# Kernel optimization log

Hardware: AMD Instinct MI355X
Metric: run time of the kernel (lower is better)

The kernel has to match this reference:

```python
import jax, jax.numpy as jnp
import numpy as np


def setup_inputs() -> dict:
    key = jax.random.key(0)
    k1, k2 = jax.random.split(key)
    B, C, H, W = 4, 256, 64, 64
    f_m = jax.random.normal(k1, (B, C, H, W), dtype=jnp.float32)
    f_d = jax.random.normal(k2, (B, C, H, W), dtype=jnp.float32)
    return {"f_m": f_m, "f_d": f_d}


def reference(f_m, f_d):
    B, C, H, W = f_d.shape
    HW = H * W
    f_fuse = f_m + f_d                      # [B, C, H, W]
    f_c = f_fuse.reshape(B, C, HW)          # [B, C, HW]
    # scores[b, n, m] = sum_c f_c[b, c, n] * f_c[b, c, m]
    scores = jnp.einsum('bcn,bcm->bnm', f_c, f_c)   # [B, HW, HW]
    att = jax.nn.softmax(scores, axis=-1)           # softmax over last dim
    f_d_r = f_d.reshape(B, C, HW)                   # [B, C, HW]
    # out[b, c, m] = sum_n f_d_r[b, c, n] * att[b, n, m]
    f_d_att = jnp.einsum('bcn,bnm->bcm', f_d_r, att).reshape(B, C, H, W)
    return f_d_att + f_d
```

## Files before the change

kernel.cpp:

```cpp
#include <hip/hip_runtime.h>
#include <math.h>

#define B_ 4
#define C_ 256
#define N_ 4096
#define LDE 68
#define LDX 72

typedef __attribute__((ext_vector_type(8))) short short8;
typedef __attribute__((ext_vector_type(4))) float f32x4;
typedef __attribute__((ext_vector_type(2))) float f32x2;

__device__ inline ushort f2bf(float f) {
    uint u = __float_as_uint(f);
    return (ushort)((u + 0x7fffu + ((u >> 16) & 1u)) >> 16);
}
__device__ inline float bf2f(ushort h) { return __uint_as_float(((uint)h) << 16); }

__device__ inline f32x4 mfma16(short8 a, short8 b, f32x4 c) {
    return __builtin_amdgcn_mfma_f32_16x16x32_bf16(a, b, c, 0, 0, 0);
}
__device__ inline f32x4 mfma8(long a, long b, f32x4 c) {
    return __builtin_amdgcn_mfma_f32_16x16x32_fp8_fp8(a, b, c, 0, 0, 0);
}

__device__ inline size_t xfi8(int b, int nt, int kk) {
    return (((size_t)(b * 256 + nt)) * 8 + kk) * 512;
}
__device__ inline size_t ffi(int b, int nc, int ct, int k2) {
    return ((((size_t)(b * 64 + nc)) * 16 + ct) * 2 + k2) * 512;
}
__device__ inline size_t eti(int b, int mt, int ng) {
    return (((size_t)(b * 256 + mt)) * 512 + (size_t)ng) * 128;
}
__device__ inline size_t zmi(int b, int nc, int mt) {
    return ((size_t)(b * 64 + nc)) * 256 + mt;
}

__global__ __launch_bounds__(256) void prep_x_kernel(const float* __restrict__ fm,
                                                     const float* __restrict__ fd,
                                                     uchar* __restrict__ xfrag8) {
    __shared__ ushort xl[64][LDX];
    const int b = blockIdx.z, c0 = blockIdx.y * 64, n0 = blockIdx.x * 64;
    const int t = threadIdx.x;
    const int n4 = (t & 15) * 4, cl = t >> 4;
    const size_t base = (size_t)b * C_ * N_;
    #pragma unroll
    for (int p = 0; p < 4; ++p) {
        const int cr = 16 * p + cl;
        const float4 m4 = *(const float4*)(fm + base + (size_t)(c0 + cr) * N_ + n0 + n4);
        const float4 d4 = *(const float4*)(fd + base + (size_t)(c0 + cr) * N_ + n0 + n4);
        ushort4 xo;
        xo.x = f2bf(m4.x + d4.x); xo.y = f2bf(m4.y + d4.y);
        xo.z = f2bf(m4.z + d4.z); xo.w = f2bf(m4.w + d4.w);
        *(ushort4*)(&xl[cr][n4]) = xo;
    }
    __syncthreads();
    const int l = t & 63, tl = t >> 6;
    const int nl = 16 * tl + (l & 15);
    #pragma unroll
    for (int j = 0; j < 2; ++j) {
        const int kk = (c0 >> 5) + j;
        const int cb = 32 * j + 8 * (l >> 4);
        float f[8];
        #pragma unroll
        for (int i = 0; i < 8; ++i) f[i] = bf2f(xl[cb + i][nl]);
        int d0 = __builtin_amdgcn_cvt_pk_fp8_f32(f[0], f[1], 0, 0);
        d0 = __builtin_amdgcn_cvt_pk_fp8_f32(f[2], f[3], d0, 1);
        int d1 = __builtin_amdgcn_cvt_pk_fp8_f32(f[4], f[5], 0, 0);
        d1 = __builtin_amdgcn_cvt_pk_fp8_f32(f[6], f[7], d1, 1);
        uint* dst = (uint*)(xfrag8 + xfi8(b, (n0 >> 4) + tl, kk) + (size_t)l * 8);
        dst[0] = (uint)d0; dst[1] = (uint)d1;
    }
}

__global__ __launch_bounds__(512, 2) void lsum_t_kernel(const uchar* __restrict__ xfrag8,
                                                        uchar* __restrict__ E8,
                                                        uchar* __restrict__ zmask,
                                                        float* __restrict__ rsbase,
                                                        float* __restrict__ rsadd,
                                                        float* __restrict__ dgall) {
    __shared__ float red[8][64];
    __shared__ float dgl[64];
    __shared__ uchar chl[34];
    __shared__ int cnt_s;
    __shared__ uint zst[34];
    const int bid = blockIdx.x;
    const int b = (bid >> 1) & 3;
    const int n0 = ((((bid >> 3) << 1) | (bid & 1))) * 64;
    const int j = n0 >> 6;
    const int t = threadIdx.x, lane = t & 63, w = t >> 6;
    const int l15 = lane & 15, q = lane >> 4;
    const int g = w >> 2, wm = w & 3;

    if (t == 0) {
        int c = 0;
        chl[c++] = (uchar)j;
        for (int k = 0; k < 64; ++k) {
            if (k == j) continue;
            const bool own = (k > j) ? (((j + k) & 1) == 0) : (((j + k) & 1) == 1);
            if (own) chl[c++] = (uchar)k;
        }
        cnt_s = c;
    }
    if (t < 34) zst[t] = 0u;

    long af[4][8];
    #pragma unroll
    for (int ns = 0; ns < 4; ++ns)
        #pragma unroll
        for (int kk = 0; kk < 8; ++kk)
            af[ns][kk] = *(const long*)(xfrag8 + xfi8(b, (n0 >> 4) + ns, kk) + (size_t)lane * 8);

    float dv[4][4];
    #pragma unroll
    for (int ns = 0; ns < 4; ++ns) {
        f32x4 dacc = {0.f, 0.f, 0.f, 0.f};
        #pragma unroll
        for (int kk = 0; kk < 8; ++kk)
            dacc = mfma8(af[ns][kk], af[ns][kk], dacc);
        #pragma unroll
        for (int r = 0; r < 4; ++r)
            dv[ns][r] = __shfl(dacc[r], 20 * q + r, 64);
    }
    if (w == 0 && l15 == 0) {
        #pragma unroll
        for (int ns = 0; ns < 4; ++ns)
            #pragma unroll
            for (int r = 0; r < 4; ++r)
                dgl[16 * ns + 4 * q + r] = dv[ns][r];
    }

    __syncthreads();
    const int cnt = cnt_s;

    long bn[8];
    {
        const int mt0 = 4 * (int)chl[g] + wm;
        #pragma unroll
        for (int kk = 0; kk < 8; ++kk)
            bn[kk] = *(const long*)(xfrag8 + xfi8(b, mt0, kk) + (size_t)lane * 8);
    }
    const size_t ebl = (size_t)l15 * 8 + 4 * (q & 1);
    const int ngb = (n0 >> 3) + (q >> 1);

    float rs[4][4] = {};
    for (int it = 0; it < 17; ++it) {
        const int idx = 2 * it + g;
        const bool valid = idx < cnt;
        const int kc = chl[valid ? idx : 0];
        const int mt = 4 * kc + wm;
        int idxn = 2 * (it + 1) + g; if (idxn >= cnt) idxn = 0;
        const int mtn = 4 * (int)chl[idxn] + wm;

        f32x4 a0 = {0.f,0.f,0.f,0.f}, a1 = {0.f,0.f,0.f,0.f};
        f32x4 a2 = {0.f,0.f,0.f,0.f}, a3 = {0.f,0.f,0.f,0.f};
        float dg0 = 0.f, dg1 = 0.f, dg2 = 0.f, dg3 = 0.f;
        __builtin_amdgcn_s_setprio(1);
        #pragma unroll
        for (int kk = 0; kk < 8; ++kk) {
            const long bc = bn[kk];
            a0 = mfma8(af[0][kk], bc, a0);
            a1 = mfma8(af[1][kk], bc, a1);
            a2 = mfma8(af[2][kk], bc, a2);
            a3 = mfma8(af[3][kk], bc, a3);
            bn[kk] = *(const long*)(xfrag8 + xfi8(b, mtn, kk) + (size_t)lane * 8);
            const uint lo = (uint)(unsigned long)bc;
            const uint hi = (uint)((unsigned long)bc >> 32);
            const f32x2 p0 = __builtin_amdgcn_cvt_pk_f32_fp8((int)lo, false);
            const f32x2 p1 = __builtin_amdgcn_cvt_pk_f32_fp8((int)lo, true);
            const f32x2 p2 = __builtin_amdgcn_cvt_pk_f32_fp8((int)hi, false);
            const f32x2 p3 = __builtin_amdgcn_cvt_pk_f32_fp8((int)hi, true);
            dg0 = fmaf(p0.x, p0.x, dg0); dg0 = fmaf(p0.y, p0.y, dg0);
            dg1 = fmaf(p1.x, p1.x, dg1); dg1 = fmaf(p1.y, p1.y, dg1);
            dg2 = fmaf(p2.x, p2.x, dg2); dg2 = fmaf(p2.y, p2.y, dg2);
            dg3 = fmaf(p3.x, p3.x, dg3); dg3 = fmaf(p3.y, p3.y, dg3);
        }
        __builtin_amdgcn_s_setprio(0);

        float df[4][4];
#define EDF(AA, NS)                                                    \
        df[NS][0] = AA[0] - dv[NS][0]; df[NS][1] = AA[1] - dv[NS][1];  \
        df[NS][2] = AA[2] - dv[NS][2]; df[NS][3] = AA[3] - dv[NS][3];
        EDF(a0, 0) EDF(a1, 1) EDF(a2, 2) EDF(a3, 3)
#undef EDF
        const float mxA = fmaxf(
            fmaxf(fmaxf(fmaxf(df[0][0], df[0][1]), fmaxf(df[0][2], df[0][3])),
                  fmaxf(fmaxf(df[1][0], df[1][1]), fmaxf(df[1][2], df[1][3]))),
            fmaxf(fmaxf(fmaxf(df[2][0], df[2][1]), fmaxf(df[2][2], df[2][3])),
                  fmaxf(fmaxf(df[3][0], df[3][1]), fmaxf(df[3][2], df[3][3]))));
        const bool nzA = valid && (__ballot(mxA > -30.0f) != 0ULL);
        if (valid && lane == 0) zmask[zmi(b, j, mt)] = nzA ? 1 : 0;
        if (nzA) {
            uint dpk[4];
#define EEXP(NS)                                                                       \
            {                                                                          \
                float e0 = __expf(df[NS][0]), e1 = __expf(df[NS][1]);                  \
                float e2 = __expf(df[NS][2]), e3 = __expf(df[NS][3]);                  \
                rs[NS][0] += e0; rs[NS][1] += e1; rs[NS][2] += e2; rs[NS][3] += e3;    \
                int d = __builtin_amdgcn_cvt_pk_fp8_f32(e0, e1, 0, 0);                 \
                d = __builtin_amdgcn_cvt_pk_fp8_f32(e2, e3, d, 1);                     \
                dpk[NS] = (uint)d;                                                     \
            }
            EEXP(0) EEXP(1) EEXP(2) EEXP(3)
#undef EEXP
            #pragma unroll
            for (int ns = 0; ns < 4; ++ns)
                *(uint*)(E8 + eti(b, mt, ngb + 2 * ns) + ebl) = dpk[ns];
        }
        if (valid && kc != j) {
            float dgm = dg0 + dg1 + dg2 + dg3;
            dgm += __shfl_xor(dgm, 16, 64);
            dgm += __shfl_xor(dgm, 32, 64);
            float dfB[4][4];
            #pragma unroll
            for (int ns = 0; ns < 4; ++ns) {
                dfB[ns][0] = (ns==0?a0[0]:ns==1?a1[0]:ns==2?a2[0]:a3[0]) - dgm;
                dfB[ns][1] = (ns==0?a0[1]:ns==1?a1[1]:ns==2?a2[1]:a3[1]) - dgm;
                dfB[ns][2] = (ns==0?a0[2]:ns==1?a1[2]:ns==2?a2[2]:a3[2]) - dgm;
                dfB[ns][3] = (ns==0?a0[3]:ns==1?a1[3]:ns==2?a2[3]:a3[3]) - dgm;
            }
            uint bits = 0;
            #pragma unroll
            for (int ns = 0; ns < 4; ++ns) {
                const float m2 = fmaxf(fmaxf(dfB[ns][0], dfB[ns][1]),
                                       fmaxf(dfB[ns][2], dfB[ns][3]));
                if (__ballot(m2 > -30.0f) != 0ULL) bits |= (1u << ns);
            }
            if (bits) {
                if (lane == 0) atomicOr(&zst[idx], bits);
                float cs = 0.f;
                #pragma unroll
                for (int ns = 0; ns < 4; ++ns)
                    #pragma unroll
                    for (int r = 0; r < 4; ++r)
                        cs += __expf(dfB[ns][r]);
                cs += __shfl_xor(cs, 16, 64);
                cs += __shfl_xor(cs, 32, 64);
                if (q == 0) atomicAdd(rsadd + b * N_ + 16 * mt + l15, cs);
            }
        }
    }
    #pragma unroll
    for (int off = 1; off < 16; off <<= 1)
        #pragma unroll
        for (int ns = 0; ns < 4; ++ns)
            #pragma unroll
            for (int r = 0; r < 4; ++r)
                rs[ns][r] += __shfl_xor(rs[ns][r], off, 64);
    if (l15 == 0) {
        #pragma unroll
        for (int ns = 0; ns < 4; ++ns)
            #pragma unroll
            for (int r = 0; r < 4; ++r)
                red[w][16 * ns + 4 * q + r] = rs[ns][r];
    }
    __syncthreads();
    if (t < 64) {
        float s = 0.f;
        #pragma unroll
        for (int ww = 0; ww < 8; ++ww) s += red[ww][t];
        rsbase[b * N_ + n0 + t] = s;
        dgall[b * N_ + n0 + t] = dgl[t];
    }
    if (t >= 64 && t < 64 + 33 * 4) {
        const int ii = (t - 64) >> 2, ns = (t - 64) & 3;
        const int idx = ii + 1;
        if (idx < cnt) {
            const int kc = chl[idx];
            zmask[zmi(b, kc, 4 * j + ns)] = (((zst[idx] >> ns) & 1u) != 0u) ? 2 : 0;
        }
    }
}

__global__ __launch_bounds__(512, 2) void out_e_kernel(const uchar* __restrict__ E8,
                                                       const uchar* __restrict__ zmask,
                                                       const float* __restrict__ rsbase,
                                                       const float* __restrict__ rsadd,
                                                       const float* __restrict__ dgall,
                                                       const uchar* __restrict__ xfrag8,
                                                       const float* __restrict__ fd32,
                                                       float* __restrict__ outp) {
    __shared__ ushort esc[8][16][66];
    const int bid = blockIdx.x;
    const int b = (bid >> 1) & 3;
    const int m0 = ((((bid >> 3) << 1) | (bid & 1))) * 64;
    const int t = threadIdx.x, lane = t & 63, w = t >> 6;
    const int l15 = lane & 15, q = lane >> 4;
    const size_t fb = (size_t)b * C_ * N_;
    const uchar* mrow = zmask + zmi(b, 0, m0 >> 4);

    f32x4 acc[2][4];
    #pragma unroll
    for (int ct = 0; ct < 2; ++ct)
        #pragma unroll
        for (int mt = 0; mt < 4; ++mt)
            acc[ct][mt] = (f32x4){0.f, 0.f, 0.f, 0.f};

    for (int gg = 0; gg < 8; ++gg) {
        uint mk[8];
        #pragma unroll
        for (int i = 0; i < 8; ++i)
            mk[i] = *(const uint*)(mrow + (size_t)(8 * gg + i) * 256);
        #pragma unroll
        for (int i = 0; i < 8; ++i) {
            const uint mki = mk[i];
            if (mki == 0) continue;
            const int nc = 8 * gg + i;
            const float* rb = rsbase + b * N_ + 64 * nc + 8 * q;
            const float* ra = rsadd + b * N_ + 64 * nc + 8 * q;
            float4 s0[2], s1[2];
            #pragma unroll
            for (int k2 = 0; k2 < 2; ++k2) {
                const float4 b0 = *(const float4*)(rb + 32 * k2);
                const float4 b1 = *(const float4*)(rb + 32 * k2 + 4);
                const float4 a0v = *(const float4*)(ra + 32 * k2);
                const float4 a1v = *(const float4*)(ra + 32 * k2 + 4);
                s0[k2].x = 1.0f / (b0.x + a0v.x); s0[k2].y = 1.0f / (b0.y + a0v.y);
                s0[k2].z = 1.0f / (b0.z + a0v.z); s0[k2].w = 1.0f / (b0.w + a0v.w);
                s1[k2].x = 1.0f / (b1.x + a1v.x); s1[k2].y = 1.0f / (b1.y + a1v.y);
                s1[k2].z = 1.0f / (b1.z + a1v.z); s1[k2].w = 1.0f / (b1.w + a1v.w);
            }
            short8 fn[2][2];
            #pragma unroll
            for (int ct = 0; ct < 2; ++ct) {
                const int c = 32 * w + 16 * ct + l15;
                const float* frow = fd32 + fb + (size_t)c * N_ + 64 * nc + 8 * q;
                #pragma unroll
                for (int k2 = 0; k2 < 2; ++k2) {
                    const float4 fa = *(const float4*)(frow + 32 * k2);
                    const float4 fb4 = *(const float4*)(frow + 32 * k2 + 4);
                    union { ushort us[8]; short8 v; } u;
                    u.us[0] = f2bf(fa.x * s0[k2].x); u.us[1] = f2bf(fa.y * s0[k2].y);
                    u.us[2] = f2bf(fa.z * s0[k2].z); u.us[3] = f2bf(fa.w * s0[k2].w);
                    u.us[4] = f2bf(fb4.x * s1[k2].x); u.us[5] = f2bf(fb4.y * s1[k2].y);
                    u.us[6] = f2bf(fb4.z * s1[k2].z); u.us[7] = f2bf(fb4.w * s1[k2].w);
                    fn[ct][k2] = u.v;
                }
            }
            if ((mki & ~0x01010101u) == 0u) {
                #pragma unroll
                for (int k2 = 0; k2 < 2; ++k2) {
                    #pragma unroll
                    for (int mt = 0; mt < 4; ++mt) {
                        if (((mki >> (8 * mt)) & 0xffu) != 1u) continue;
                        const long e8 = *(const long*)(E8 + eti(b, (m0 >> 4) + mt, 8 * nc + 4 * k2 + q) + (size_t)l15 * 8);
                        const uint lo = (uint)(unsigned long)e8;
                        const uint hi = (uint)((unsigned long)e8 >> 32);
                        const f32x2 f01 = __builtin_amdgcn_cvt_pk_f32_fp8((int)lo, false);
                        const f32x2 f23 = __builtin_amdgcn_cvt_pk_f32_fp8((int)lo, true);
                        const f32x2 f45 = __builtin_amdgcn_cvt_pk_f32_fp8((int)hi, false);
                        const f32x2 f67 = __builtin_amdgcn_cvt_pk_f32_fp8((int)hi, true);
                        union { uint u[4]; short8 v; } be;
                        asm("v_cvt_pk_bf16_f32 %0, %1, %2" : "=v"(be.u[0]) : "v"(f01.x), "v"(f01.y));
                        asm("v_cvt_pk_bf16_f32 %0, %1, %2" : "=v"(be.u[1]) : "v"(f23.x), "v"(f23.y));
                        asm("v_cvt_pk_bf16_f32 %0, %1, %2" : "=v"(be.u[2]) : "v"(f45.x), "v"(f45.y));
                        asm("v_cvt_pk_bf16_f32 %0, %1, %2" : "=v"(be.u[3]) : "v"(f67.x), "v"(f67.y));
                        acc[0][mt] = mfma16(fn[0][k2], be.v, acc[0][mt]);
                        acc[1][mt] = mfma16(fn[1][k2], be.v, acc[1][mt]);
                    }
                }
            } else {
                #pragma unroll
                for (int mt = 0; mt < 4; ++mt) {
                    long bmf[8];
                    #pragma unroll
                    for (int kk = 0; kk < 8; ++kk)
                        bmf[kk] = *(const long*)(xfrag8 + xfi8(b, (m0 >> 4) + mt, kk) + (size_t)lane * 8);
                    #pragma unroll
                    for (int nt = 0; nt < 4; ++nt) {
                        long anf[8];
                        #pragma unroll
                        for (int kk = 0; kk < 8; ++kk)
                            anf[kk] = *(const long*)(xfrag8 + xfi8(b, 4 * nc + nt, kk) + (size_t)lane * 8);
                        f32x4 sacc = {0.f, 0.f, 0.f, 0.f};
                        #pragma unroll
                        for (int kk = 0; kk < 8; ++kk)
                            sacc = mfma8(anf[kk], bmf[kk], sacc);
                        #pragma unroll
                        for (int r = 0; r < 4; ++r) {
                            const float gv = dgall[b * N_ + 64 * nc + 16 * nt + 4 * q + r];
                            esc[w][l15][16 * nt + 4 * q + r] = f2bf(__expf(sacc[r] - gv));
                        }
                    }
                    #pragma unroll
                    for (int k2 = 0; k2 < 2; ++k2) {
                        const short8 be = *(const short8*)(&esc[w][l15][32 * k2 + 8 * q]);
                        acc[0][mt] = mfma16(fn[0][k2], be, acc[0][mt]);
                        acc[1][mt] = mfma16(fn[1][k2], be, acc[1][mt]);
                    }
                }
            }
        }
    }
    #pragma unroll
    for (int ct = 0; ct < 2; ++ct)
        #pragma unroll
        for (int mt = 0; mt < 4; ++mt)
            #pragma unroll
            for (int r = 0; r < 4; ++r) {
                const int c = 32 * w + 16 * ct + 4 * q + r;
                const int m = m0 + 16 * mt + l15;
                const size_t o = fb + (size_t)c * N_ + m;
                outp[o] = acc[ct][mt][r] + fd32[o];
            }
}

__global__ __launch_bounds__(256) void prep_kernel(const float* __restrict__ fm,
                                                   const float* __restrict__ fd,
                                                   uchar* __restrict__ xfrag8,
                                                   ushort* __restrict__ ffrag) {
    __shared__ ushort xl[64][LDX];
    __shared__ ushort fl[64][LDX];
    const int b = blockIdx.z, c0 = blockIdx.y * 64, n0 = blockIdx.x * 64;
    const int t = threadIdx.x;
    const int n4 = (t & 15) * 4, cl = t >> 4;
    const size_t base = (size_t)b * C_ * N_;
    #pragma unroll
    for (int p = 0; p < 4; ++p) {
        const int cr = 16 * p + cl;
        const float4 m4 = *(const float4*)(fm + base + (size_t)(c0 + cr) * N_ + n0 + n4);
        const float4 d4 = *(const float4*)(fd + base + (size_t)(c0 + cr) * N_ + n0 + n4);
        ushort4 fo;
        fo.x = f2bf(d4.x); fo.y = f2bf(d4.y); fo.z = f2bf(d4.z); fo.w = f2bf(d4.w);
        *(ushort4*)(&fl[cr][n4]) = fo;
        ushort4 xo;
        xo.x = f2bf(m4.x + d4.x); xo.y = f2bf(m4.y + d4.y);
        xo.z = f2bf(m4.z + d4.z); xo.w = f2bf(m4.w + d4.w);
        *(ushort4*)(&xl[cr][n4]) = xo;
    }
    __syncthreads();
    const int l = t & 63, tl = t >> 6;
    {
        const int nl = 16 * tl + (l & 15);
        #pragma unroll
        for (int j = 0; j < 2; ++j) {
            const int kk = (c0 >> 5) + j;
            const int cb = 32 * j + 8 * (l >> 4);
            float f[8];
            #pragma unroll
            for (int i = 0; i < 8; ++i) f[i] = bf2f(xl[cb + i][nl]);
            int d0 = __builtin_amdgcn_cvt_pk_fp8_f32(f[0], f[1], 0, 0);
            d0 = __builtin_amdgcn_cvt_pk_fp8_f32(f[2], f[3], d0, 1);
            int d1 = __builtin_amdgcn_cvt_pk_fp8_f32(f[4], f[5], 0, 0);
            d1 = __builtin_amdgcn_cvt_pk_fp8_f32(f[6], f[7], d1, 1);
            uint* dst = (uint*)(xfrag8 + xfi8(b, (n0 >> 4) + tl, kk) + (size_t)l * 8);
            dst[0] = (uint)d0; dst[1] = (uint)d1;
        }
    }
    {
        const int row = 16 * tl + (l & 15);
        #pragma unroll
        for (int k2 = 0; k2 < 2; ++k2) {
            const int col = 32 * k2 + 8 * (l >> 4);
            const ushort4 a0 = *(const ushort4*)(&fl[row][col]);
            const ushort4 a1 = *(const ushort4*)(&fl[row][col + 4]);
            ushort* dst = ffrag + ffi(b, n0 >> 6, (c0 >> 4) + tl, k2) + l * 8;
            *(ushort4*)(dst) = a0; *(ushort4*)(dst + 4) = a1;
        }
    }
}

__global__ __launch_bounds__(512, 2) void lsum_g_kernel(const uchar* __restrict__ xfrag8,
                                                        float* __restrict__ lg) {
    __shared__ float red[8][64];
    __shared__ float dgl[64];
    const int bid = blockIdx.x;
    const int b = (bid >> 1) & 3;
    const int n0 = ((((bid >> 3) << 1) | (bid & 1))) * 64;
    const int t = threadIdx.x, lane = t & 63, w = t >> 6;
    const int l15 = lane & 15, q = lane >> 4;

    long af[4][8];
    #pragma unroll
    for (int ns = 0; ns < 4; ++ns)
        #pragma unroll
        for (int kk = 0; kk < 8; ++kk)
            af[ns][kk] = *(const long*)(xfrag8 + xfi8(b, (n0 >> 4) + ns, kk) + (size_t)lane * 8);

    float dv[4][4];
    #pragma unroll
    for (int ns = 0; ns < 4; ++ns) {
        f32x4 dacc = {0.f, 0.f, 0.f, 0.f};
        #pragma unroll
        for (int kk = 0; kk < 8; ++kk)
            dacc = mfma8(af[ns][kk], af[ns][kk], dacc);
        #pragma unroll
        for (int r = 0; r < 4; ++r)
            dv[ns][r] = __shfl(dacc[r], 20 * q + r, 64);
    }
    if (w == 0 && l15 == 0) {
        #pragma unroll
        for (int ns = 0; ns < 4; ++ns)
            #pragma unroll
            for (int r = 0; r < 4; ++r)
                dgl[16 * ns + 4 * q + r] = dv[ns][r];
    }

    long bn[8];
    #pragma unroll
    for (int kk = 0; kk < 8; ++kk)
        bn[kk] = *(const long*)(xfrag8 + xfi8(b, w, kk) + (size_t)lane * 8);

    float rs[4][4] = {};
    for (int mc = 0; mc < 32; ++mc) {
        const int mtn = (mc + 1 < 32) ? (mc + 1) * 8 + w : w;
        f32x4 a0 = {0.f,0.f,0.f,0.f}, a1 = {0.f,0.f,0.f,0.f};
        f32x4 a2 = {0.f,0.f,0.f,0.f}, a3 = {0.f,0.f,0.f,0.f};
        #pragma unroll
        for (int kk = 0; kk < 8; ++kk) {
            const long bc = bn[kk];
            a0 = mfma8(af[0][kk], bc, a0);
            a1 = mfma8(af[1][kk], bc, a1);
            a2 = mfma8(af[2][kk], bc, a2);
            a3 = mfma8(af[3][kk], bc, a3);
            bn[kk] = *(const long*)(xfrag8 + xfi8(b, mtn, kk) + (size_t)lane * 8);
        }
        #pragma unroll
        for (int r = 0; r < 4; ++r) {
            rs[0][r] += __expf(a0[r] - dv[0][r]);
            rs[1][r] += __expf(a1[r] - dv[1][r]);
            rs[2][r] += __expf(a2[r] - dv[2][r]);
            rs[3][r] += __expf(a3[r] - dv[3][r]);
        }
    }
    #pragma unroll
    for (int off = 1; off < 16; off <<= 1)
        #pragma unroll
        for (int ns = 0; ns < 4; ++ns)
            #pragma unroll
            for (int r = 0; r < 4; ++r)
                rs[ns][r] += __shfl_xor(rs[ns][r], off, 64);
    if (l15 == 0) {
        #pragma unroll
        for (int ns = 0; ns < 4; ++ns)
            #pragma unroll
            for (int r = 0; r < 4; ++r)
                red[w][16 * ns + 4 * q + r] = rs[ns][r];
    }
    __syncthreads();
    if (t < 64) {
        float s = 0.f;
        #pragma unroll
        for (int ww = 0; ww < 8; ++ww) s += red[ww][t];
        lg[b * N_ + n0 + t] = dgl[t] + __logf(s);
    }
}

__global__ __launch_bounds__(512, 2) void out_g_kernel(const uchar* __restrict__ xfrag8,
                                                       const ushort* __restrict__ ffrag,
                                                       const float* __restrict__ gg,
                                                       const float* __restrict__ fd32,
                                                       float* __restrict__ outp) {
    __shared__ ushort ET[2][64][LDE];
    const int bid = blockIdx.x;
    const int b = (bid >> 1) & 3;
    const int m0 = ((((bid >> 3) << 1) | (bid & 1))) * 64;
    const int t = threadIdx.x, lane = t & 63, w = t >> 6;
    const int l15 = lane & 15, q = lane >> 4;
    const int a = w & 3, h = w >> 2;
    const size_t fb = (size_t)b * C_ * N_;

    long bfr[2][8];
    #pragma unroll
    for (int jt = 0; jt < 2; ++jt)
        #pragma unroll
        for (int kk = 0; kk < 8; ++kk)
            bfr[jt][kk] = *(const long*)(xfrag8 + xfi8(b, (m0 >> 4) + 2 * h + jt, kk) + (size_t)lane * 8);

    f32x4 acc[2][4];
    #pragma unroll
    for (int ct = 0; ct < 2; ++ct)
        #pragma unroll
        for (int mt = 0; mt < 4; ++mt)
            acc[ct][mt] = (f32x4){0.f, 0.f, 0.f, 0.f};

    long an[8];
    #pragma unroll
    for (int kk = 0; kk < 8; ++kk)
        an[kk] = *(const long*)(xfrag8 + xfi8(b, a, kk) + (size_t)lane * 8);
    float gn[4];
    #pragma unroll
    for (int r = 0; r < 4; ++r) gn[r] = gg[b * N_ + 16 * a + 4 * q + r];

    int p = 0;
    for (int n0c = 0; n0c < N_; n0c += 64, p ^= 1) {
        const int nc = n0c >> 6;
        short8 fn[2][2];
        #pragma unroll
        for (int ct = 0; ct < 2; ++ct)
            #pragma unroll
            for (int k2 = 0; k2 < 2; ++k2)
                fn[ct][k2] = *(const short8*)(ffrag + ffi(b, nc, 2 * w + ct, k2) + lane * 8);
        float gv[4];
        #pragma unroll
        for (int r = 0; r < 4; ++r) gv[r] = gn[r];
        const int nx = (n0c + 64 < N_) ? n0c + 64 : 0;
        #pragma unroll
        for (int r = 0; r < 4; ++r) gn[r] = gg[b * N_ + nx + 16 * a + 4 * q + r];

        f32x4 s0 = {0.f, 0.f, 0.f, 0.f}, s1 = {0.f, 0.f, 0.f, 0.f};
        #pragma unroll
        for (int kk = 0; kk < 8; ++kk) {
            s0 = mfma8(an[kk], bfr[0][kk], s0);
            s1 = mfma8(an[kk], bfr[1][kk], s1);
            an[kk] = *(const long*)(xfrag8 + xfi8(b, (nx >> 4) + a, kk) + (size_t)lane * 8);
        }
        ushort4 e0, e1;
        e0.x = f2bf(__expf(s0[0] - gv[0])); e0.y = f2bf(__expf(s0[1] - gv[1]));
        e0.z = f2bf(__expf(s0[2] - gv[2])); e0.w = f2bf(__expf(s0[3] - gv[3]));
        e1.x = f2bf(__expf(s1[0] - gv[0])); e1.y = f2bf(__expf(s1[1] - gv[1]));
        e1.z = f2bf(__expf(s1[2] - gv[2])); e1.w = f2bf(__expf(s1[3] - gv[3]));
        *(ushort4*)(&ET[p][32 * h + l15][16 * a + 4 * q])      = e0;
        *(ushort4*)(&ET[p][32 * h + 16 + l15][16 * a + 4 * q]) = e1;

        asm volatile("s_waitcnt lgkmcnt(0)\n\ts_barrier" ::: "memory");

        #pragma unroll
        for (int k2 = 0; k2 < 2; ++k2) {
            #pragma unroll
            for (int mt = 0; mt < 4; ++mt) {
                const short8 be = *(const short8*)(&ET[p][16 * mt + l15][32 * k2 + 8 * q]);
                acc[0][mt] = mfma16(fn[0][k2], be, acc[0][mt]);
                acc[1][mt] = mfma16(fn[1][k2], be, acc[1][mt]);
            }
        }
    }
    #pragma unroll
    for (int ct = 0; ct < 2; ++ct)
        #pragma unroll
        for (int mt = 0; mt < 4; ++mt)
            #pragma unroll
            for (int r = 0; r < 4; ++r) {
                const int c = 32 * w + 16 * ct + 4 * q + r;
                const int m = m0 + 16 * mt + l15;
                const size_t o = fb + (size_t)c * N_ + m;
                outp[o] = acc[ct][mt][r] + fd32[o];
            }
}

extern "C" void kernel_launch(void* const* d_in, const int* in_sizes, int n_in,
                              void* d_out, int out_size, void* d_ws, size_t ws_size,
                              hipStream_t stream) {
    const float* fm = (const float*)d_in[0];
    const float* fd = (const float*)d_in[1];
    float* outp = (float*)d_out;

    const size_t xb_elts = (size_t)B_ * N_ * C_;
    const size_t e_bytes = (size_t)B_ * N_ * N_;
    const size_t z_bytes = (size_t)B_ * 64 * 256;
    const size_t f_bytes = (size_t)B_ * N_ * 4;
    const size_t need_e  = xb_elts + e_bytes + z_bytes + 3 * f_bytes;
    const size_t need_g  = xb_elts * 3 + f_bytes;

    uchar* xfrag8 = (uchar*)d_ws;

    if (ws_size >= need_e) {
        uchar* E8     = xfrag8 + xb_elts;
        uchar* zmask  = E8 + e_bytes;
        float* rsbase = (float*)(zmask + z_bytes);
        float* rsadd  = rsbase + (size_t)B_ * N_;
        float* dgall  = rsadd + (size_t)B_ * N_;
        hipMemsetAsync(rsadd, 0, f_bytes, stream);
        prep_x_kernel<<<dim3(N_ / 64, C_ / 64, B_), 256, 0, stream>>>(fm, fd, xfrag8);
        lsum_t_kernel<<<dim3(256), 512, 0, stream>>>(xfrag8, E8, zmask, rsbase, rsadd, dgall);
        out_e_kernel<<<dim3(256), 512, 0, stream>>>(E8, zmask, rsbase, rsadd, dgall, xfrag8, fd, outp);
    } else if (ws_size >= need_g) {
        ushort* ffrag = (ushort*)(xfrag8 + xb_elts);
        float*  lg    = (float*)(xfrag8 + xb_elts * 3);
        prep_kernel<<<dim3(N_ / 64, C_ / 64, B_), 256, 0, stream>>>(fm, fd, xfrag8, ffrag);
        lsum_g_kernel<<<dim3(256), 512, 0, stream>>>(xfrag8, lg);
        out_g_kernel<<<dim3(256), 512, 0, stream>>>(xfrag8, ffrag, lg, fd, outp);
    }
}
```

Before: 115.1 us.

## Precompute Gram diagonal in separate kernel and drop per-tile dequant reductions

Adds a small dg_kernel that computes the diagonal self-dot-products (row norms) for all positions with MFMA and also zeroes rsadd, which replaces the hipMemsetAsync. lsum_t_kernel now reads the diagonal from global memory instead of recomputing it from its A fragments, and drops the per-iteration fp8 unpack plus FMA reduction of the B-tile norms. It instead prefetches each column tile's diagonal value one iteration ahead. This removes ALU work from the inner MFMA loop at the cost of an extra kernel launch and a dependency on global reads.

```diff
diff --git a/kernel.cpp b/kernel.cpp
--- a/kernel.cpp
+++ b/kernel.cpp
@@ -74,14 +74,41 @@
     }
 }
 
+__global__ __launch_bounds__(256) void dg_kernel(const uchar* __restrict__ xfrag8,
+                                                 float* __restrict__ dgall,
+                                                 float* __restrict__ rsadd) {
+    const int t = threadIdx.x, lane = t & 63, w = t >> 6;
+    const int tid = blockIdx.x * 4 + w;
+    const int b = tid >> 8, nt = tid & 255;
+    const int l15 = lane & 15, q = lane >> 4;
+    long af[8];
+    #pragma unroll
+    for (int kk = 0; kk < 8; ++kk)
+        af[kk] = *(const long*)(xfrag8 + xfi8(b, nt, kk) + (size_t)lane * 8);
+    f32x4 dacc = {0.f, 0.f, 0.f, 0.f};
+    #pragma unroll
+    for (int kk = 0; kk < 8; ++kk)
+        dacc = mfma8(af[kk], af[kk], dacc);
+    float dvv[4];
+    #pragma unroll
+    for (int r = 0; r < 4; ++r)
+        dvv[r] = __shfl(dacc[r], 20 * q + r, 64);
+    if (l15 == 0) {
+        #pragma unroll
+        for (int r = 0; r < 4; ++r)
+            dgall[b * N_ + 16 * nt + 4 * q + r] = dvv[r];
+    }
+    const int zi = blockIdx.x * 256 + t;
+    if (zi < B_ * N_) rsadd[zi] = 0.f;
+}
+
 __global__ __launch_bounds__(512, 2) void lsum_t_kernel(const uchar* __restrict__ xfrag8,
+                                                        const float* __restrict__ dgall,
                                                         uchar* __restrict__ E8,
                                                         uchar* __restrict__ zmask,
                                                         float* __restrict__ rsbase,
-                                                        float* __restrict__ rsadd,
-                                                        float* __restrict__ dgall) {
+                                                        float* __restrict__ rsadd) {
     __shared__ float red[8][64];
-    __shared__ float dgl[64];
     __shared__ uchar chl[34];
     __shared__ int cnt_s;
     __shared__ uint zst[34];
@@ -114,32 +141,22 @@
 
     float dv[4][4];
     #pragma unroll
-    for (int ns = 0; ns < 4; ++ns) {
-        f32x4 dacc = {0.f, 0.f, 0.f, 0.f};
-        #pragma unroll
-        for (int kk = 0; kk < 8; ++kk)
-            dacc = mfma8(af[ns][kk], af[ns][kk], dacc);
+    for (int ns = 0; ns < 4; ++ns)
         #pragma unroll
         for (int r = 0; r < 4; ++r)
-            dv[ns][r] = __shfl(dacc[r], 20 * q + r, 64);
-    }
-    if (w == 0 && l15 == 0) {
-        #pragma unroll
-        for (int ns = 0; ns < 4; ++ns)
-            #pragma unroll
-            for (int r = 0; r < 4; ++r)
-                dgl[16 * ns + 4 * q + r] = dv[ns][r];
-    }
+            dv[ns][r] = dgall[b * N_ + n0 + 16 * ns + 4 * q + r];
 
     __syncthreads();
     const int cnt = cnt_s;
 
     long bn[8];
+    float dgm_cur;
     {
         const int mt0 = 4 * (int)chl[g] + wm;
         #pragma unroll
         for (int kk = 0; kk < 8; ++kk)
             bn[kk] = *(const long*)(xfrag8 + xfi8(b, mt0, kk) + (size_t)lane * 8);
+        dgm_cur = dgall[b * N_ + 16 * mt0 + l15];
     }
     const size_t ebl = (size_t)l15 * 8 + 4 * (q & 1);
     const int ngb = (n0 >> 3) + (q >> 1);
@@ -155,7 +172,6 @@
 
         f32x4 a0 = {0.f,0.f,0.f,0.f}, a1 = {0.f,0.f,0.f,0.f};
         f32x4 a2 = {0.f,0.f,0.f,0.f}, a3 = {0.f,0.f,0.f,0.f};
-        float dg0 = 0.f, dg1 = 0.f, dg2 = 0.f, dg3 = 0.f;
         __builtin_amdgcn_s_setprio(1);
         #pragma unroll
         for (int kk = 0; kk < 8; ++kk) {
@@ -165,18 +181,10 @@
             a2 = mfma8(af[2][kk], bc, a2);
             a3 = mfma8(af[3][kk], bc, a3);
             bn[kk] = *(const long*)(xfrag8 + xfi8(b, mtn, kk) + (size_t)lane * 8);
-            const uint lo = (uint)(unsigned long)bc;
-            const uint hi = (uint)((unsigned long)bc >> 32);
-            const f32x2 p0 = __builtin_amdgcn_cvt_pk_f32_fp8((int)lo, false);
-            const f32x2 p1 = __builtin_amdgcn_cvt_pk_f32_fp8((int)lo, true);
-            const f32x2 p2 = __builtin_amdgcn_cvt_pk_f32_fp8((int)hi, false);
-            const f32x2 p3 = __builtin_amdgcn_cvt_pk_f32_fp8((int)hi, true);
-            dg0 = fmaf(p0.x, p0.x, dg0); dg0 = fmaf(p0.y, p0.y, dg0);
-            dg1 = fmaf(p1.x, p1.x, dg1); dg1 = fmaf(p1.y, p1.y, dg1);
-            dg2 = fmaf(p2.x, p2.x, dg2); dg2 = fmaf(p2.y, p2.y, dg2);
-            dg3 = fmaf(p3.x, p3.x, dg3); dg3 = fmaf(p3.y, p3.y, dg3);
         }
         __builtin_amdgcn_s_setprio(0);
+        const float dgm = dgm_cur;
+        dgm_cur = dgall[b * N_ + 16 * mtn + l15];
 
         float df[4][4];
 #define EDF(AA, NS)                                                    \
@@ -209,9 +217,6 @@
                 *(uint*)(E8 + eti(b, mt, ngb + 2 * ns) + ebl) = dpk[ns];
         }
         if (valid && kc != j) {
-            float dgm = dg0 + dg1 + dg2 + dg3;
-            dgm += __shfl_xor(dgm, 16, 64);
-            dgm += __shfl_xor(dgm, 32, 64);
             float dfB[4][4];
             #pragma unroll
             for (int ns = 0; ns < 4; ++ns) {
@@ -261,7 +266,6 @@
         #pragma unroll
         for (int ww = 0; ww < 8; ++ww) s += red[ww][t];
         rsbase[b * N_ + n0 + t] = s;
-        dgall[b * N_ + n0 + t] = dgl[t];
     }
     if (t >= 64 && t < 64 + 33 * 4) {
         const int ii = (t - 64) >> 2, ns = (t - 64) & 3;
@@ -661,9 +665,9 @@
         float* rsbase = (float*)(zmask + z_bytes);
         float* rsadd  = rsbase + (size_t)B_ * N_;
         float* dgall  = rsadd + (size_t)B_ * N_;
-        hipMemsetAsync(rsadd, 0, f_bytes, stream);
         prep_x_kernel<<<dim3(N_ / 64, C_ / 64, B_), 256, 0, stream>>>(fm, fd, xfrag8);
-        lsum_t_kernel<<<dim3(256), 512, 0, stream>>>(xfrag8, E8, zmask, rsbase, rsadd, dgall);
+        dg_kernel<<<dim3(256), 256, 0, stream>>>(xfrag8, dgall, rsadd);
+        lsum_t_kernel<<<dim3(256), 512, 0, stream>>>(xfrag8, dgall, E8, zmask, rsbase, rsadd);
         out_e_kernel<<<dim3(256), 512, 0, stream>>>(E8, zmask, rsbase, rsadd, dgall, xfrag8, fd, outp);
     } else if (ws_size >= need_g) {
         ushort* ffrag = (ushort*)(xfrag8 + xb_elts);
```

After: 111.2 us. 1.03x faster.
